# Performance work log

Measured on AMD Instinct MI355X. Metric: run time of the kernel, lower is better.

## Reference

```python
import jax, jax.numpy as jnp
import numpy as np

N_EMBD = 1024
N_HEAD = 16
HEAD_SIZE = N_EMBD // N_HEAD
SEQ_LEN = 2048


def setup_inputs() -> dict:
    key = jax.random.key(0)
    k_x, k_wa, k_ba, k_wp, k_bp = jax.random.split(key, 5)
    s = 0.02
    return {
        "x": jax.random.normal(k_x, (4, SEQ_LEN, N_EMBD), dtype=jnp.float32),
        "w_attn": jax.random.normal(k_wa, (N_EMBD, 3 * N_EMBD), dtype=jnp.float32) * s,
        "b_attn": jax.random.normal(k_ba, (3 * N_EMBD,), dtype=jnp.float32) * s,
        "w_proj": jax.random.normal(k_wp, (N_EMBD, N_EMBD), dtype=jnp.float32) * s,
        "b_proj": jax.random.normal(k_bp, (N_EMBD,), dtype=jnp.float32) * s,
    }


def reference(x, w_attn, b_attn, w_proj, b_proj):
    B, T, C = x.shape
    H, D = N_HEAD, HEAD_SIZE
    qkv = x @ w_attn + b_attn                      # [B,T,3C]
    q, k, v = jnp.split(qkv, 3, axis=-1)
    q = q.reshape(B, T, H, D).transpose(0, 2, 1, 3)  # [B,H,T,D]
    k = k.reshape(B, T, H, D).transpose(0, 2, 1, 3)
    v = v.reshape(B, T, H, D).transpose(0, 2, 1, 3)
    att = jnp.einsum('bhqd,bhkd->bhqk', q, k) / jnp.sqrt(jnp.float32(D))
    causal = jnp.tril(jnp.ones((T, T), dtype=bool))
    att = jnp.where(causal[None, None], att, jnp.float32(-jnp.inf))
    att = jax.nn.softmax(att, axis=-1)
    out = jnp.einsum('bhqk,bhkd->bhqd', att, v)    # [B,H,T,D]
    out = out.transpose(0, 2, 1, 3).reshape(B, T, C)
    return out @ w_proj + b_proj
```

## Files before the change

### kernel.cpp

```cpp
#include <hip/hip_runtime.h>

typedef short short8 __attribute__((ext_vector_type(8)));
typedef short short4v __attribute__((ext_vector_type(4)));
typedef float f32x4 __attribute__((ext_vector_type(4)));
typedef unsigned uint2v __attribute__((ext_vector_type(2)));

__device__ __forceinline__ float bf2f(short b) {
  unsigned u = ((unsigned)(unsigned short)b) << 16;
  return __builtin_bit_cast(float, u);
}
__device__ __forceinline__ short f2bf(float f) {
  unsigned u = __builtin_bit_cast(unsigned, f);
  u += 0x7fffu + ((u >> 16) & 1u);
  return (short)(u >> 16);
}
__device__ __forceinline__ unsigned cvt_pk_bf16(float lo, float hi) {
  unsigned r;
  asm("v_cvt_pk_bf16_f32 %0, %1, %2" : "=v"(r) : "v"(lo), "v"(hi));
  return r;
}

__device__ __forceinline__ void gload_lds16(const void* g, void* l) {
  __builtin_amdgcn_global_load_lds(
      (const __attribute__((address_space(1))) unsigned int*)g,
      (__attribute__((address_space(3))) unsigned int*)l, 16, 0, 0);
}

__global__ __launch_bounds__(256) void k_convert_bf16(const float* __restrict__ in,
                                                      short* __restrict__ out, int n8) {
  int i = blockIdx.x * 256 + threadIdx.x;
  if (i >= n8) return;
  const float4* p = (const float4*)in;
  float4 a = p[2 * i], b = p[2 * i + 1];
  short8 o;
  o[0] = f2bf(a.x); o[1] = f2bf(a.y); o[2] = f2bf(a.z); o[3] = f2bf(a.w);
  o[4] = f2bf(b.x); o[5] = f2bf(b.y); o[6] = f2bf(b.z); o[7] = f2bf(b.w);
  ((short8*)out)[i] = o;
}

__global__ __launch_bounds__(256) void k_transpose_w(const float* __restrict__ w,
                                                     short* __restrict__ wT, int K, int N) {
  __shared__ float t[32][33];
  int nt = N >> 5;
  int rt = blockIdx.x / nt, ct = blockIdx.x % nt;
  int tx = threadIdx.x & 31, ty = threadIdx.x >> 5;
#pragma unroll
  for (int i = 0; i < 4; ++i) {
    int r = ty * 4 + i;
    t[r][tx] = w[(size_t)(rt * 32 + r) * N + ct * 32 + tx];
  }
  __syncthreads();
#pragma unroll
  for (int i = 0; i < 4; ++i) {
    int r = ty * 4 + i;
    wT[(size_t)(ct * 32 + r) * K + rt * 32 + tx] = f2bf(t[tx][r]);
  }
}

template <bool BF16OUT>
__global__ __launch_bounds__(256) void k_gemm_bt(const short* __restrict__ A,
                                                 const short* __restrict__ Bt,
                                                 const float* __restrict__ bias,
                                                 void* __restrict__ Cout,
                                                 int M, int N, int K) {
  __shared__ __align__(16) short As[128 * 32];
  __shared__ __align__(16) short Bs[128 * 32];
  int nt = N >> 7;
  int mt = blockIdx.x / nt, ct = blockIdx.x % nt;
  int tid = threadIdx.x, w = tid >> 6, lane = tid & 63;
  int l15 = lane & 15, l4 = lane >> 4;
  int wr = (w >> 1) * 64, wc = (w & 1) * 64;
  const short* Abase = A + (size_t)mt * 128 * K;
  const short* Bbase = Bt + (size_t)ct * 128 * K;
  f32x4 acc[4][4];
#pragma unroll
  for (int m = 0; m < 4; ++m)
#pragma unroll
    for (int n = 0; n < 4; ++n) acc[m][n] = f32x4{0.f, 0.f, 0.f, 0.f};

  for (int kt = 0; kt < K; kt += 32) {
    __syncthreads();
#pragma unroll
    for (int i = 0; i < 2; ++i) {
      int idx = (w * 2 + i) * 64 + lane;
      gload_lds16(Abase + (size_t)(idx >> 2) * K + kt + (idx & 3) * 8, &As[(w * 2 + i) * 512]);
      gload_lds16(Bbase + (size_t)(idx >> 2) * K + kt + (idx & 3) * 8, &Bs[(w * 2 + i) * 512]);
    }
    __syncthreads();
    short8 af[4], bfr[4];
#pragma unroll
    for (int m = 0; m < 4; ++m) af[m] = *(const short8*)&As[(wr + m * 16 + l15) * 32 + l4 * 8];
#pragma unroll
    for (int n = 0; n < 4; ++n) bfr[n] = *(const short8*)&Bs[(wc + n * 16 + l15) * 32 + l4 * 8];
#pragma unroll
    for (int m = 0; m < 4; ++m)
#pragma unroll
      for (int n = 0; n < 4; ++n)
        acc[m][n] = __builtin_amdgcn_mfma_f32_16x16x32_bf16(af[m], bfr[n], acc[m][n], 0, 0, 0);
  }

#pragma unroll
  for (int m = 0; m < 4; ++m) {
#pragma unroll
    for (int n = 0; n < 4; ++n) {
      int row = mt * 128 + wr + m * 16 + l4 * 4;
      int col = ct * 128 + wc + n * 16 + l15;
      float bv = bias[col];
#pragma unroll
      for (int j = 0; j < 4; ++j) {
        float v = acc[m][n][j] + bv;
        if constexpr (BF16OUT)
          ((short*)Cout)[(size_t)(row + j) * N + col] = f2bf(v);
        else
          ((float*)Cout)[(size_t)(row + j) * N + col] = v;
      }
    }
  }
}

__global__ __launch_bounds__(256) void k_transpose_v(const short* __restrict__ qkv,
                                                     short* __restrict__ vT) {
  __shared__ __align__(16) short t[64][72];
  int blk = blockIdx.x;
  int tt = blk & 31, bh = blk >> 5;
  int batch = bh >> 4, h = bh & 15;
  int tid = threadIdx.x;
  const short* base = qkv + (size_t)(batch * 2048 + tt * 64) * 3072 + 2048 + h * 64;
#pragma unroll
  for (int rep = 0; rep < 2; ++rep) {
    int idx = rep * 256 + tid;
    int r = idx >> 3, dc = idx & 7;
    *(short8*)&t[r][dc * 8] = *(const short8*)(base + (size_t)r * 3072 + dc * 8);
  }
  __syncthreads();
  short* obase = vT + (size_t)bh * 64 * 2048 + tt * 64;
#pragma unroll
  for (int rep = 0; rep < 2; ++rep) {
    int idx = rep * 256 + tid;
    int d = idx >> 3, tc = idx & 7;
    short8 o;
#pragma unroll
    for (int i = 0; i < 8; ++i) o[i] = t[tc * 8 + i][d];
    *(short8*)(obase + (size_t)d * 2048 + tc * 8) = o;
  }
}

__global__ __launch_bounds__(256, 2) void k_attn(const short* __restrict__ qkv,
                                                 const short* __restrict__ vT,
                                                 short* __restrict__ out) {
  constexpr int T = 2048, C3 = 3072;
  __shared__ __align__(16) short Kl[2][64 * 72];
  __shared__ __align__(16) short P_lds[4][32 * 72];
  int bp = blockIdx.x & 7, bh = blockIdx.x >> 3;
  int batch = bh >> 4, h = bh & 15;
  int tid = threadIdx.x, w = tid >> 6, lane = tid & 63;
  int l15 = lane & 15, l4 = lane >> 4;

  int qt[2];
  qt[0] = 63 - (bp * 4 + w);
  qt[1] = bp * 4 + w;
  int lim[2] = {qt[0] >> 1, qt[1] >> 1};
  int ktb = (63 - bp * 4) >> 1;

  const short* kbase = qkv + (size_t)(batch * T) * C3 + 1024 + h * 64;
  const short* vbase = vT + (size_t)bh * 64 * T;

  int sr0 = tid >> 3, sr1 = 32 + (tid >> 3), sdc = (tid & 7) * 8;

  const float SCL = 0.18033688f;
  short8 qf[2][2][2];
#pragma unroll
  for (int t = 0; t < 2; ++t)
#pragma unroll
    for (int qc = 0; qc < 2; ++qc) {
      const short* qrow = qkv + (size_t)(batch * T + qt[t] * 32 + qc * 16 + l15) * C3 + h * 64;
#pragma unroll
      for (int kc = 0; kc < 2; ++kc) {
        short8 v = *(const short8*)(qrow + kc * 32 + l4 * 8);
#pragma unroll
        for (int i = 0; i < 8; ++i) v[i] = f2bf(bf2f(v[i]) * SCL);
        qf[t][qc][kc] = v;
      }
    }

  f32x4 o_[2][2][4];
  float l_[2][2];
#pragma unroll
  for (int t = 0; t < 2; ++t)
#pragma unroll
    for (int qc = 0; qc < 2; ++qc) {
      l_[t][qc] = 0.f;
#pragma unroll
      for (int dt = 0; dt < 4; ++dt) o_[t][qc][dt] = f32x4{0.f, 0.f, 0.f, 0.f};
    }

  {
    short8 a = *(const short8*)(kbase + (size_t)sr0 * C3 + sdc);
    short8 b = *(const short8*)(kbase + (size_t)sr1 * C3 + sdc);
    *(short8*)&Kl[0][sr0 * 72 + sdc] = a;
    *(short8*)&Kl[0][sr1 * 72 + sdc] = b;
  }
  __syncthreads();

  int cur = 0;
  for (int kt = 0; kt <= ktb; ++kt) {
    bool more = (kt < ktb);
    bool act0 = (kt <= lim[0]), act1 = (kt <= lim[1]);

    short8 pre0, pre1;
    if (more) {
      pre0 = *(const short8*)(kbase + (size_t)((kt + 1) * 64 + sr0) * C3 + sdc);
      pre1 = *(const short8*)(kbase + (size_t)((kt + 1) * 64 + sr1) * C3 + sdc);
    }

    const short* Kb = &Kl[cur][0];
    short8 kf[4][2];
#pragma unroll
    for (int kvt = 0; kvt < 4; ++kvt)
#pragma unroll
      for (int kc = 0; kc < 2; ++kc)
        kf[kvt][kc] = *(const short8*)(Kb + (kvt * 16 + l15) * 72 + kc * 32 + l4 * 8);

    short8 vf[4][2];
#pragma unroll
    for (int dt = 0; dt < 4; ++dt)
#pragma unroll
      for (int kc = 0; kc < 2; ++kc)
        vf[dt][kc] = *(const short8*)(vbase + (size_t)(dt * 16 + l15) * T + kt * 64 + kc * 32 + l4 * 8);

#pragma unroll
    for (int t = 0; t < 2; ++t) {
      bool act = (t == 0) ? act0 : act1;
      if (!act) continue;
      short* pb = &P_lds[w][0];

#pragma unroll
      for (int qc = 0; qc < 2; ++qc) {
        f32x4 s[4];
#pragma unroll
        for (int kvt = 0; kvt < 4; ++kvt) s[kvt] = f32x4{0.f, 0.f, 0.f, 0.f};
        __builtin_amdgcn_s_setprio(1);
#pragma unroll
        for (int kvt = 0; kvt < 4; ++kvt)
#pragma unroll
          for (int kc = 0; kc < 2; ++kc)
            s[kvt] = __builtin_amdgcn_mfma_f32_16x16x32_bf16(kf[kvt][kc], qf[t][qc][kc], s[kvt], 0, 0, 0);
        __builtin_amdgcn_s_setprio(0);

        if (kt == lim[t]) {
          int qg = qt[t] * 32 + qc * 16 + l15;
#pragma unroll
          for (int kvt = 0; kvt < 4; ++kvt)
#pragma unroll
            for (int j = 0; j < 4; ++j) {
              int kg = kt * 64 + kvt * 16 + l4 * 4 + j;
              if (kg > qg) s[kvt][j] = -1e30f;
            }
        }

        float ls = 0.f;
#pragma unroll
        for (int kvt = 0; kvt < 4; ++kvt) {
          float p0 = exp2f(s[kvt][0]);
          float p1 = exp2f(s[kvt][1]);
          float p2 = exp2f(s[kvt][2]);
          float p3 = exp2f(s[kvt][3]);
          ls += (p0 + p1) + (p2 + p3);
          unsigned lo = cvt_pk_bf16(p0, p1);
          unsigned hi = cvt_pk_bf16(p2, p3);
          *(uint2v*)(pb + (qc * 16 + l15) * 72 + kvt * 16 + l4 * 4) = uint2v{lo, hi};
        }
        l_[t][qc] += ls;
      }

      asm volatile("s_waitcnt lgkmcnt(0)" ::: "memory");

      __builtin_amdgcn_s_setprio(1);
#pragma unroll
      for (int qc = 0; qc < 2; ++qc)
#pragma unroll
        for (int dt = 0; dt < 4; ++dt)
#pragma unroll
          for (int kc = 0; kc < 2; ++kc) {
            short8 pf = *(const short8*)(pb + (qc * 16 + l15) * 72 + kc * 32 + l4 * 8);
            o_[t][qc][dt] = __builtin_amdgcn_mfma_f32_16x16x32_bf16(vf[dt][kc], pf, o_[t][qc][dt], 0, 0, 0);
          }
      __builtin_amdgcn_s_setprio(0);
    }

    if (more) {
      *(short8*)&Kl[cur ^ 1][sr0 * 72 + sdc] = pre0;
      *(short8*)&Kl[cur ^ 1][sr1 * 72 + sdc] = pre1;
    }
    __syncthreads();
    cur ^= 1;
  }

#pragma unroll
  for (int t = 0; t < 2; ++t) {
#pragma unroll
    for (int qc = 0; qc < 2; ++qc) {
      float lt = l_[t][qc];
      lt += __shfl_xor(lt, 16);
      lt += __shfl_xor(lt, 32);
      float inv = 1.f / lt;
      size_t rowb = (size_t)(batch * T + qt[t] * 32 + qc * 16 + l15) * 1024 + h * 64;
#pragma unroll
      for (int dt = 0; dt < 4; ++dt) {
        short4v pk4;
#pragma unroll
        for (int j = 0; j < 4; ++j) pk4[j] = f2bf(o_[t][qc][dt][j] * inv);
        *(short4v*)(out + rowb + dt * 16 + l4 * 4) = pk4;
      }
    }
  }
}

extern "C" void kernel_launch(void* const* d_in, const int* in_sizes, int n_in,
                              void* d_out, int out_size, void* d_ws, size_t ws_size,
                              hipStream_t stream) {
  const float* x      = (const float*)d_in[0];
  const float* w_attn = (const float*)d_in[1];
  const float* b_attn = (const float*)d_in[2];
  const float* w_proj = (const float*)d_in[3];
  const float* b_proj = (const float*)d_in[4];
  float* out = (float*)d_out;

  char* ws = (char*)d_ws;
  short* xb   = (short*)(ws);
  short* waT  = (short*)(ws + 16777216);
  short* wpT  = (short*)(ws + 23068672);
  short* qkv  = (short*)(ws + 25165824);
  short* vT   = (short*)(ws + 75497472);
  short* attn = xb;

  k_convert_bf16<<<4096, 256, 0, stream>>>(x, xb, 1048576);
  k_transpose_w<<<32 * 96, 256, 0, stream>>>(w_attn, waT, 1024, 3072);
  k_transpose_w<<<32 * 32, 256, 0, stream>>>(w_proj, wpT, 1024, 1024);
  k_gemm_bt<true><<<64 * 24, 256, 0, stream>>>(xb, waT, b_attn, qkv, 8192, 3072, 1024);
  k_transpose_v<<<2048, 256, 0, stream>>>(qkv, vT);
  k_attn<<<512, 256, 0, stream>>>(qkv, vT, attn);
  k_gemm_bt<false><<<64 * 8, 256, 0, stream>>>(attn, wpT, b_proj, out, 8192, 1024, 1024);
}
```

Baseline: 203.3 us.

## Load K directly from global per wave and compute row sums with MFMA

Result: slower. 246.7 us (+21.3%).

```diff
diff --git a/kernel.cpp b/kernel.cpp
--- a/kernel.cpp
+++ b/kernel.cpp
@@ -149,7 +149,6 @@
                                                  const short* __restrict__ vT,
                                                  short* __restrict__ out) {
   constexpr int T = 2048, C3 = 3072;
-  __shared__ __align__(16) short Kl[2][64 * 72];
   __shared__ __align__(16) short P_lds[4][32 * 72];
   int bp = blockIdx.x & 7, bh = blockIdx.x >> 3;
   int batch = bh >> 4, h = bh & 15;
@@ -160,12 +159,9 @@
   qt[0] = 63 - (bp * 4 + w);
   qt[1] = bp * 4 + w;
   int lim[2] = {qt[0] >> 1, qt[1] >> 1};
-  int ktb = (63 - bp * 4) >> 1;
 
   const short* kbase = qkv + (size_t)(batch * T) * C3 + 1024 + h * 64;
   const short* vbase = vT + (size_t)bh * 64 * T;
-
-  int sr0 = tid >> 3, sr1 = 32 + (tid >> 3), sdc = (tid & 7) * 8;
 
   const float SCL = 0.18033688f;
   short8 qf[2][2][2];
@@ -183,43 +179,33 @@
       }
     }
 
+  const f32x4 ZERO = f32x4{0.f, 0.f, 0.f, 0.f};
+  short8 ONES;
+#pragma unroll
+  for (int i = 0; i < 8; ++i) ONES[i] = (short)0x3F80;
+
   f32x4 o_[2][2][4];
-  float l_[2][2];
+  f32x4 lacc[2][2];
 #pragma unroll
   for (int t = 0; t < 2; ++t)
 #pragma unroll
     for (int qc = 0; qc < 2; ++qc) {
-      l_[t][qc] = 0.f;
-#pragma unroll
-      for (int dt = 0; dt < 4; ++dt) o_[t][qc][dt] = f32x4{0.f, 0.f, 0.f, 0.f};
-    }
-
-  {
-    short8 a = *(const short8*)(kbase + (size_t)sr0 * C3 + sdc);
-    short8 b = *(const short8*)(kbase + (size_t)sr1 * C3 + sdc);
-    *(short8*)&Kl[0][sr0 * 72 + sdc] = a;
-    *(short8*)&Kl[0][sr1 * 72 + sdc] = b;
-  }
-  __syncthreads();
-
-  int cur = 0;
-  for (int kt = 0; kt <= ktb; ++kt) {
-    bool more = (kt < ktb);
-    bool act0 = (kt <= lim[0]), act1 = (kt <= lim[1]);
-
-    short8 pre0, pre1;
-    if (more) {
-      pre0 = *(const short8*)(kbase + (size_t)((kt + 1) * 64 + sr0) * C3 + sdc);
-      pre1 = *(const short8*)(kbase + (size_t)((kt + 1) * 64 + sr1) * C3 + sdc);
-    }
-
-    const short* Kb = &Kl[cur][0];
+      lacc[t][qc] = ZERO;
+#pragma unroll
+      for (int dt = 0; dt < 4; ++dt) o_[t][qc][dt] = ZERO;
+    }
+
+  short* pb = &P_lds[w][0];
+
+  for (int kt = 0; kt <= lim[0]; ++kt) {
+    bool act1 = (kt <= lim[1]);
+
     short8 kf[4][2];
 #pragma unroll
     for (int kvt = 0; kvt < 4; ++kvt)
 #pragma unroll
       for (int kc = 0; kc < 2; ++kc)
-        kf[kvt][kc] = *(const short8*)(Kb + (kvt * 16 + l15) * 72 + kc * 32 + l4 * 8);
+        kf[kvt][kc] = *(const short8*)(kbase + (size_t)(kt * 64 + kvt * 16 + l15) * C3 + kc * 32 + l4 * 8);
 
     short8 vf[4][2];
 #pragma unroll
@@ -230,21 +216,17 @@
 
 #pragma unroll
     for (int t = 0; t < 2; ++t) {
-      bool act = (t == 0) ? act0 : act1;
-      if (!act) continue;
-      short* pb = &P_lds[w][0];
+      if (t == 1 && !act1) continue;
 
 #pragma unroll
       for (int qc = 0; qc < 2; ++qc) {
         f32x4 s[4];
-#pragma unroll
-        for (int kvt = 0; kvt < 4; ++kvt) s[kvt] = f32x4{0.f, 0.f, 0.f, 0.f};
         __builtin_amdgcn_s_setprio(1);
 #pragma unroll
-        for (int kvt = 0; kvt < 4; ++kvt)
-#pragma unroll
-          for (int kc = 0; kc < 2; ++kc)
-            s[kvt] = __builtin_amdgcn_mfma_f32_16x16x32_bf16(kf[kvt][kc], qf[t][qc][kc], s[kvt], 0, 0, 0);
+        for (int kvt = 0; kvt < 4; ++kvt) {
+          s[kvt] = __builtin_amdgcn_mfma_f32_16x16x32_bf16(kf[kvt][0], qf[t][qc][0], ZERO, 0, 0, 0);
+          s[kvt] = __builtin_amdgcn_mfma_f32_16x16x32_bf16(kf[kvt][1], qf[t][qc][1], s[kvt], 0, 0, 0);
+        }
         __builtin_amdgcn_s_setprio(0);
 
         if (kt == lim[t]) {
@@ -258,19 +240,16 @@
             }
         }
 
-        float ls = 0.f;
 #pragma unroll
         for (int kvt = 0; kvt < 4; ++kvt) {
           float p0 = exp2f(s[kvt][0]);
           float p1 = exp2f(s[kvt][1]);
           float p2 = exp2f(s[kvt][2]);
           float p3 = exp2f(s[kvt][3]);
-          ls += (p0 + p1) + (p2 + p3);
           unsigned lo = cvt_pk_bf16(p0, p1);
           unsigned hi = cvt_pk_bf16(p2, p3);
           *(uint2v*)(pb + (qc * 16 + l15) * 72 + kvt * 16 + l4 * 4) = uint2v{lo, hi};
         }
-        l_[t][qc] += ls;
       }
 
       asm volatile("s_waitcnt lgkmcnt(0)" ::: "memory");
@@ -279,31 +258,22 @@
 #pragma unroll
       for (int qc = 0; qc < 2; ++qc)
 #pragma unroll
-        for (int dt = 0; dt < 4; ++dt)
-#pragma unroll
-          for (int kc = 0; kc < 2; ++kc) {
-            short8 pf = *(const short8*)(pb + (qc * 16 + l15) * 72 + kc * 32 + l4 * 8);
+        for (int kc = 0; kc < 2; ++kc) {
+          short8 pf = *(const short8*)(pb + (qc * 16 + l15) * 72 + kc * 32 + l4 * 8);
+          lacc[t][qc] = __builtin_amdgcn_mfma_f32_16x16x32_bf16(ONES, pf, lacc[t][qc], 0, 0, 0);
+#pragma unroll
+          for (int dt = 0; dt < 4; ++dt)
             o_[t][qc][dt] = __builtin_amdgcn_mfma_f32_16x16x32_bf16(vf[dt][kc], pf, o_[t][qc][dt], 0, 0, 0);
-          }
+        }
       __builtin_amdgcn_s_setprio(0);
     }
-
-    if (more) {
-      *(short8*)&Kl[cur ^ 1][sr0 * 72 + sdc] = pre0;
-      *(short8*)&Kl[cur ^ 1][sr1 * 72 + sdc] = pre1;
-    }
-    __syncthreads();
-    cur ^= 1;
   }
 
 #pragma unroll
   for (int t = 0; t < 2; ++t) {
 #pragma unroll
     for (int qc = 0; qc < 2; ++qc) {
-      float lt = l_[t][qc];
-      lt += __shfl_xor(lt, 16);
-      lt += __shfl_xor(lt, 32);
-      float inv = 1.f / lt;
+      float inv = 1.f / lacc[t][qc][0];
       size_t rowb = (size_t)(batch * T + qt[t] * 32 + qc * 16 + l15) * 1024 + h * 64;
 #pragma unroll
       for (int dt = 0; dt < 4; ++dt) {
```

## Replace GEMM with 256x128-tile, 4-stage pipelined, swizzled-LDS kernel

Applied to the files above, without the earlier changes.

Measured after the change: 219.4 us. 1.08x slower.

```diff
diff --git a/kernel.cpp b/kernel.cpp
--- a/kernel.cpp
+++ b/kernel.cpp
@@ -58,53 +58,91 @@
 }
 
 template <bool BF16OUT>
-__global__ __launch_bounds__(256) void k_gemm_bt(const short* __restrict__ A,
-                                                 const short* __restrict__ Bt,
-                                                 const float* __restrict__ bias,
-                                                 void* __restrict__ Cout,
-                                                 int M, int N, int K) {
-  __shared__ __align__(16) short As[128 * 32];
-  __shared__ __align__(16) short Bs[128 * 32];
+__global__ __launch_bounds__(512, 1) void k_gemm256(const short* __restrict__ A,
+                                                    const short* __restrict__ Bt,
+                                                    const float* __restrict__ bias,
+                                                    void* __restrict__ Cout,
+                                                    int M, int N, int K) {
+  __shared__ __align__(16) short Ab[4][256 * 32];
+  __shared__ __align__(16) short Bb[4][128 * 32];
   int nt = N >> 7;
-  int mt = blockIdx.x / nt, ct = blockIdx.x % nt;
+  int nwg = gridDim.x;
+  int bid = blockIdx.x;
+  int swz = (bid & 7) * (nwg >> 3) + (bid >> 3);
+  int mt = swz / nt, ct = swz % nt;
   int tid = threadIdx.x, w = tid >> 6, lane = tid & 63;
   int l15 = lane & 15, l4 = lane >> 4;
-  int wr = (w >> 1) * 64, wc = (w & 1) * 64;
-  const short* Abase = A + (size_t)mt * 128 * K;
+  int wm = w >> 2, wn = w & 3;
+  const short* Abase = A + (size_t)mt * 256 * K;
   const short* Bbase = Bt + (size_t)ct * 128 * K;
-  f32x4 acc[4][4];
-#pragma unroll
-  for (int m = 0; m < 4; ++m)
-#pragma unroll
-    for (int n = 0; n < 4; ++n) acc[m][n] = f32x4{0.f, 0.f, 0.f, 0.f};
-
-  for (int kt = 0; kt < K; kt += 32) {
-    __syncthreads();
+  int NT = K >> 5;
+
+  int la = lane >> 2, lc = lane & 3;
+
+  auto stage = [&](int kt, int b) {
 #pragma unroll
     for (int i = 0; i < 2; ++i) {
-      int idx = (w * 2 + i) * 64 + lane;
-      gload_lds16(Abase + (size_t)(idx >> 2) * K + kt + (idx & 3) * 8, &As[(w * 2 + i) * 512]);
-      gload_lds16(Bbase + (size_t)(idx >> 2) * K + kt + (idx & 3) * 8, &Bs[(w * 2 + i) * 512]);
-    }
-    __syncthreads();
-    short8 af[4], bfr[4];
-#pragma unroll
-    for (int m = 0; m < 4; ++m) af[m] = *(const short8*)&As[(wr + m * 16 + l15) * 32 + l4 * 8];
-#pragma unroll
-    for (int n = 0; n < 4; ++n) bfr[n] = *(const short8*)&Bs[(wc + n * 16 + l15) * 32 + l4 * 8];
-#pragma unroll
-    for (int m = 0; m < 4; ++m)
-#pragma unroll
-      for (int n = 0; n < 4; ++n)
+      int ra = i * 128 + w * 16 + la;
+      gload_lds16(Abase + (size_t)ra * K + kt * 32 + ((lc ^ ((ra >> 1) & 3)) * 8),
+                  &Ab[b][i * 4096 + w * 512]);
+    }
+    int rb = w * 16 + la;
+    gload_lds16(Bbase + (size_t)rb * K + kt * 32 + ((lc ^ ((rb >> 1) & 3)) * 8),
+                &Bb[b][w * 512]);
+  };
+
+  f32x4 acc[8][2];
+#pragma unroll
+  for (int m = 0; m < 8; ++m)
+#pragma unroll
+    for (int n = 0; n < 2; ++n) acc[m][n] = f32x4{0.f, 0.f, 0.f, 0.f};
+
+  stage(0, 0);
+  stage(1, 1);
+  stage(2, 2);
+  asm volatile("s_waitcnt vmcnt(6)" ::: "memory");
+  __builtin_amdgcn_s_barrier();
+  __builtin_amdgcn_sched_barrier(0);
+
+  int koff = (l4 * 8) ^ (((l15 >> 1) & 3) << 3);
+
+  for (int kt = 0; kt < NT; ++kt) {
+    int b = kt & 3;
+    if (kt + 3 < NT) stage(kt + 3, (kt + 3) & 3);
+
+    short8 af[8], bfr[2];
+#pragma unroll
+    for (int m = 0; m < 8; ++m)
+      af[m] = *(const short8*)&Ab[b][(wm * 128 + m * 16 + l15) * 32 + koff];
+#pragma unroll
+    for (int n = 0; n < 2; ++n)
+      bfr[n] = *(const short8*)&Bb[b][(wn * 32 + n * 16 + l15) * 32 + koff];
+
+    __builtin_amdgcn_s_setprio(1);
+#pragma unroll
+    for (int m = 0; m < 8; ++m)
+#pragma unroll
+      for (int n = 0; n < 2; ++n)
         acc[m][n] = __builtin_amdgcn_mfma_f32_16x16x32_bf16(af[m], bfr[n], acc[m][n], 0, 0, 0);
-  }
-
-#pragma unroll
-  for (int m = 0; m < 4; ++m) {
-#pragma unroll
-    for (int n = 0; n < 4; ++n) {
-      int row = mt * 128 + wr + m * 16 + l4 * 4;
-      int col = ct * 128 + wc + n * 16 + l15;
+    __builtin_amdgcn_s_setprio(0);
+
+    if (kt + 3 < NT) {
+      asm volatile("s_waitcnt vmcnt(6)" ::: "memory");
+    } else if (kt + 2 < NT) {
+      asm volatile("s_waitcnt vmcnt(3)" ::: "memory");
+    } else if (kt + 1 < NT) {
+      asm volatile("s_waitcnt vmcnt(0)" ::: "memory");
+    }
+    __builtin_amdgcn_s_barrier();
+    __builtin_amdgcn_sched_barrier(0);
+  }
+
+#pragma unroll
+  for (int m = 0; m < 8; ++m) {
+#pragma unroll
+    for (int n = 0; n < 2; ++n) {
+      int row = mt * 256 + wm * 128 + m * 16 + l4 * 4;
+      int col = ct * 128 + wn * 32 + n * 16 + l15;
       float bv = bias[col];
 #pragma unroll
       for (int j = 0; j < 4; ++j) {
@@ -337,8 +375,8 @@
   k_convert_bf16<<<4096, 256, 0, stream>>>(x, xb, 1048576);
   k_transpose_w<<<32 * 96, 256, 0, stream>>>(w_attn, waT, 1024, 3072);
   k_transpose_w<<<32 * 32, 256, 0, stream>>>(w_proj, wpT, 1024, 1024);
-  k_gemm_bt<true><<<64 * 24, 256, 0, stream>>>(xb, waT, b_attn, qkv, 8192, 3072, 1024);
+  k_gemm256<true><<<768, 512, 0, stream>>>(xb, waT, b_attn, qkv, 8192, 3072, 1024);
   k_transpose_v<<<2048, 256, 0, stream>>>(qkv, vT);
   k_attn<<<512, 256, 0, stream>>>(qkv, vT, attn);
-  k_gemm_bt<false><<<64 * 8, 256, 0, stream>>>(attn, wpT, b_proj, out, 8192, 1024, 1024);
-}
+  k_gemm256<false><<<256, 512, 0, stream>>>(attn, wpT, b_proj, out, 8192, 1024, 1024);
+}
```

## Replace QKV GEMM with 256x256 8-wave ping-pong pipelined MFMA kernel

Applied to the files above, without the earlier changes.

Result: faster. 199.1 us (-2.1%).

```diff
diff --git a/kernel.cpp b/kernel.cpp
--- a/kernel.cpp
+++ b/kernel.cpp
@@ -24,6 +24,11 @@
   __builtin_amdgcn_global_load_lds(
       (const __attribute__((address_space(1))) unsigned int*)g,
       (__attribute__((address_space(3))) unsigned int*)l, 16, 0, 0);
+}
+
+__device__ __forceinline__ short8 lds_frag(const short* tile, int row, int kc, int l4) {
+  int chunk = (kc * 4 + l4) ^ (row & 7);
+  return *(const short8*)&tile[row * 64 + chunk * 8];
 }
 
 __global__ __launch_bounds__(256) void k_convert_bf16(const float* __restrict__ in,
@@ -54,6 +59,170 @@
   for (int i = 0; i < 4; ++i) {
     int r = ty * 4 + i;
     wT[(size_t)(ct * 32 + r) * K + rt * 32 + tx] = f2bf(t[tx][r]);
+  }
+}
+
+template <bool BF16OUT>
+__global__ __launch_bounds__(512, 1) void k_gemm8p(const short* __restrict__ A,
+                                                   const short* __restrict__ Bt,
+                                                   const float* __restrict__ bias,
+                                                   void* __restrict__ Cout,
+                                                   int M, int N, int K) {
+  __shared__ __align__(16) short Ab[2][256 * 64];
+  __shared__ __align__(16) short Bb[2][256 * 64];
+  int nt = N >> 8;
+  int nwg = gridDim.x;
+  int bid = blockIdx.x;
+  int swz = (bid & 7) * (nwg >> 3) + (bid >> 3);
+  int mt = swz / nt, ct = swz % nt;
+  int tid = threadIdx.x, w = tid >> 6, lane = tid & 63;
+  int l15 = lane & 15, l4 = lane >> 4;
+  int wm = w >> 2, wn = w & 3;
+  const short* Abase = A + (size_t)mt * 256 * K;
+  const short* Bbase = Bt + (size_t)ct * 256 * K;
+  int NT = K >> 6;
+
+  int srow = lane >> 3;
+  int slc = (lane & 7) ^ srow;
+
+  auto stage = [&](const short* gbase, short* dstTile, int kt, int half) {
+#pragma unroll
+    for (int i = 0; i < 2; ++i) {
+      int rowg = half * 128 + i * 64 + w * 8;
+      gload_lds16(gbase + (size_t)(rowg + srow) * K + kt * 64 + slc * 8,
+                  dstTile + (size_t)rowg * 64);
+    }
+  };
+
+  f32x4 acc[8][4];
+#pragma unroll
+  for (int m = 0; m < 8; ++m)
+#pragma unroll
+    for (int n = 0; n < 4; ++n) acc[m][n] = f32x4{0.f, 0.f, 0.f, 0.f};
+
+  stage(Bbase, &Bb[0][0], 0, 0);
+  stage(Bbase, &Bb[0][0], 0, 1);
+  stage(Abase, &Ab[0][0], 0, 0);
+  stage(Abase, &Ab[0][0], 0, 1);
+  stage(Bbase, &Bb[1][0], 1, 0);
+  stage(Bbase, &Bb[1][0], 1, 1);
+  stage(Abase, &Ab[1][0], 1, 0);
+  stage(Abase, &Ab[1][0], 1, 1);
+  asm volatile("s_waitcnt vmcnt(8)" ::: "memory");
+  __builtin_amdgcn_s_barrier();
+
+  for (int t = 0; t < NT; ++t) {
+    int b = t & 1;
+    const short* At = &Ab[b][0];
+    const short* Btl = &Bb[b][0];
+    short* Aw = &Ab[b][0];
+    short* Bw = &Bb[b][0];
+    bool pre = (t + 2 < NT);
+
+    short8 aflo[4][2], bflo[2][2], bfhi[2][2], afhi[4][2];
+#pragma unroll
+    for (int mq = 0; mq < 4; ++mq)
+#pragma unroll
+      for (int kc = 0; kc < 2; ++kc)
+        aflo[mq][kc] = lds_frag(At, wm * 128 + mq * 16 + l15, kc, l4);
+#pragma unroll
+    for (int nq = 0; nq < 2; ++nq)
+#pragma unroll
+      for (int kc = 0; kc < 2; ++kc)
+        bflo[nq][kc] = lds_frag(Btl, wn * 64 + nq * 16 + l15, kc, l4);
+    __builtin_amdgcn_s_barrier();
+    asm volatile("s_waitcnt lgkmcnt(0)" ::: "memory");
+    __builtin_amdgcn_sched_barrier(0);
+    __builtin_amdgcn_s_setprio(1);
+#pragma unroll
+    for (int mq = 0; mq < 4; ++mq)
+#pragma unroll
+      for (int nq = 0; nq < 2; ++nq)
+#pragma unroll
+        for (int kc = 0; kc < 2; ++kc)
+          acc[mq][nq] = __builtin_amdgcn_mfma_f32_16x16x32_bf16(aflo[mq][kc], bflo[nq][kc], acc[mq][nq], 0, 0, 0);
+    __builtin_amdgcn_s_setprio(0);
+    __builtin_amdgcn_s_barrier();
+
+#pragma unroll
+    for (int nq = 0; nq < 2; ++nq)
+#pragma unroll
+      for (int kc = 0; kc < 2; ++kc)
+        bfhi[nq][kc] = lds_frag(Btl, wn * 64 + 32 + nq * 16 + l15, kc, l4);
+    __builtin_amdgcn_s_barrier();
+    asm volatile("s_waitcnt lgkmcnt(0)" ::: "memory");
+    __builtin_amdgcn_sched_barrier(0);
+    __builtin_amdgcn_s_setprio(1);
+#pragma unroll
+    for (int mq = 0; mq < 4; ++mq)
+#pragma unroll
+      for (int nq = 0; nq < 2; ++nq)
+#pragma unroll
+        for (int kc = 0; kc < 2; ++kc)
+          acc[mq][2 + nq] = __builtin_amdgcn_mfma_f32_16x16x32_bf16(aflo[mq][kc], bfhi[nq][kc], acc[mq][2 + nq], 0, 0, 0);
+    __builtin_amdgcn_s_setprio(0);
+    __builtin_amdgcn_s_barrier();
+
+#pragma unroll
+    for (int mq = 0; mq < 4; ++mq)
+#pragma unroll
+      for (int kc = 0; kc < 2; ++kc)
+        afhi[mq][kc] = lds_frag(At, wm * 128 + 64 + mq * 16 + l15, kc, l4);
+    if (pre) {
+      stage(Bbase, Bw, t + 2, 0);
+      stage(Bbase, Bw, t + 2, 1);
+    }
+    __builtin_amdgcn_s_barrier();
+    asm volatile("s_waitcnt lgkmcnt(0)" ::: "memory");
+    __builtin_amdgcn_sched_barrier(0);
+    __builtin_amdgcn_s_setprio(1);
+#pragma unroll
+    for (int mq = 0; mq < 4; ++mq)
+#pragma unroll
+      for (int nq = 0; nq < 2; ++nq)
+#pragma unroll
+        for (int kc = 0; kc < 2; ++kc)
+          acc[4 + mq][2 + nq] = __builtin_amdgcn_mfma_f32_16x16x32_bf16(afhi[mq][kc], bfhi[nq][kc], acc[4 + mq][2 + nq], 0, 0, 0);
+    __builtin_amdgcn_s_setprio(0);
+    __builtin_amdgcn_s_barrier();
+
+    if (pre) {
+      stage(Abase, Aw, t + 2, 0);
+      stage(Abase, Aw, t + 2, 1);
+    }
+    __builtin_amdgcn_s_setprio(1);
+#pragma unroll
+    for (int mq = 0; mq < 4; ++mq)
+#pragma unroll
+      for (int nq = 0; nq < 2; ++nq)
+#pragma unroll
+        for (int kc = 0; kc < 2; ++kc)
+          acc[4 + mq][nq] = __builtin_amdgcn_mfma_f32_16x16x32_bf16(afhi[mq][kc], bflo[nq][kc], acc[4 + mq][nq], 0, 0, 0);
+    __builtin_amdgcn_s_setprio(0);
+    if (pre) {
+      asm volatile("s_waitcnt vmcnt(8)" ::: "memory");
+    } else if (t + 1 < NT) {
+      asm volatile("s_waitcnt vmcnt(0)" ::: "memory");
+    }
+    __builtin_amdgcn_s_barrier();
+  }
+
+#pragma unroll
+  for (int m = 0; m < 8; ++m) {
+#pragma unroll
+    for (int n = 0; n < 4; ++n) {
+      int row = mt * 256 + wm * 128 + m * 16 + l4 * 4;
+      int col = ct * 256 + wn * 64 + n * 16 + l15;
+      float bv = bias[col];
+#pragma unroll
+      for (int j = 0; j < 4; ++j) {
+        float v = acc[m][n][j] + bv;
+        if constexpr (BF16OUT)
+          ((short*)Cout)[(size_t)(row + j) * N + col] = f2bf(v);
+        else
+          ((float*)Cout)[(size_t)(row + j) * N + col] = v;
+      }
+    }
   }
 }
 
@@ -337,7 +506,7 @@
   k_convert_bf16<<<4096, 256, 0, stream>>>(x, xb, 1048576);
   k_transpose_w<<<32 * 96, 256, 0, stream>>>(w_attn, waT, 1024, 3072);
   k_transpose_w<<<32 * 32, 256, 0, stream>>>(w_proj, wpT, 1024, 1024);
-  k_gemm_bt<true><<<64 * 24, 256, 0, stream>>>(xb, waT, b_attn, qkv, 8192, 3072, 1024);
+  k_gemm8p<true><<<384, 512, 0, stream>>>(xb, waT, b_attn, qkv, 8192, 3072, 1024);
   k_transpose_v<<<2048, 256, 0, stream>>>(qkv, vT);
   k_attn<<<512, 256, 0, stream>>>(qkv, vT, attn);
   k_gemm_bt<false><<<64 * 8, 256, 0, stream>>>(attn, wpT, b_proj, out, 8192, 1024, 1024);
```
